# Performance work log

Measured on AMD Instinct MI355X. Metric: run time of the kernel, lower is better.

Reference implementation:

```python
import jax, jax.numpy as jnp
import numpy as np

N = 50000      # nodes
E = 800000     # edges (avg degree 16)
F_IN = 128     # input feature dim
HID = 64       # hidden_channels
HEADS = 2
NEG_SLOPE = 0.2


def setup_inputs() -> dict:
    key = jax.random.key(0)
    ks = jax.random.split(key, 20)
    w = lambda k, shape: jax.random.normal(k, shape, jnp.float32) * 0.1
    inp = {
        "x": jax.random.normal(ks[0], (N, F_IN), jnp.float32),
        "edge_index": jax.random.randint(ks[1], (2, E), 0, N, dtype=jnp.int32),
    }
    # layer specs: (in_dim, heads) ; out per head = HID
    specs = [(F_IN, HEADS), (HID * HEADS, HEADS), (HID * HEADS, HEADS), (HID * HEADS, 1)]
    ki = 2
    for i, (fin, h) in enumerate(specs, 1):
        inp[f"Wl{i}"] = w(ks[ki], (fin, h * HID)); ki += 1
        inp[f"Wr{i}"] = w(ks[ki], (fin, h * HID)); ki += 1
        inp[f"att{i}"] = w(ks[ki], (h, HID)); ki += 1
        inp[f"b{i}"] = jnp.zeros((h * HID,), jnp.float32)
    return inp


def gat_layer(x, src, dst, Wl, Wr, att, b):
    # GATv2Conv: e_ij = att . LeakyReLU(Wl x_j + Wr x_i), softmax over incoming edges of i
    H, C = att.shape
    n = x.shape[0]
    xl = (x @ Wl).reshape(n, H, C)   # source-side transform
    xr = (x @ Wr).reshape(n, H, C)   # target-side transform
    e = jax.nn.leaky_relu(xl[src] + xr[dst], negative_slope=NEG_SLOPE)  # [E,H,C]
    score = jnp.einsum('ehc,hc->eh', e, att)                            # [E,H]
    # segment softmax over destination nodes
    m = jax.ops.segment_max(score, dst, num_segments=n)
    m = jnp.where(jnp.isfinite(m), m, 0.0)  # nodes with no in-edges
    ex = jnp.exp(score - m[dst])
    den = jax.ops.segment_sum(ex, dst, num_segments=n)
    alpha = ex / (den[dst] + 1e-16)                                     # [E,H]
    out = jax.ops.segment_sum(xl[src] * alpha[:, :, None], dst, num_segments=n)  # [N,H,C]
    return out.reshape(n, H * C) + b


def reference(x, edge_index, Wl1, Wr1, att1, b1, Wl2, Wr2, att2, b2,
              Wl3, Wr3, att3, b3, Wl4, Wr4, att4, b4):
    src, dst = edge_index[0], edge_index[1]
    x = jax.nn.relu(gat_layer(x, src, dst, Wl1, Wr1, att1, b1))
    x = jax.nn.relu(gat_layer(x, src, dst, Wl2, Wr2, att2, b2))
    x = jax.nn.relu(gat_layer(x, src, dst, Wl3, Wr3, att3, b3))
    return gat_layer(x, src, dst, Wl4, Wr4, att4, b4)  # [N, HID]
```

## Files before the change

kernel.cpp:

```cpp
#include <hip/hip_runtime.h>
#include <hip/hip_fp16.h>
#include <math.h>
#include <limits.h>

#define FIN 128
#define NEG_SLOPE 0.2f

typedef _Float16 f16x8 __attribute__((ext_vector_type(8)));
typedef float f32x4 __attribute__((ext_vector_type(4)));
typedef float f32x2 __attribute__((ext_vector_type(2)));

static __device__ __forceinline__ f32x2 pk_add(f32x2 a, f32x2 b) {
    f32x2 d; asm("v_pk_add_f32 %0, %1, %2" : "=v"(d) : "v"(a), "v"(b)); return d;
}
static __device__ __forceinline__ f32x2 pk_fma(f32x2 a, f32x2 b, f32x2 c) {
    f32x2 d; asm("v_pk_fma_f32 %0, %1, %2, %3" : "=v"(d) : "v"(a), "v"(b), "v"(c)); return d;
}

static __device__ __forceinline__ f32x2 h2f2x(unsigned int u) {
    __half2 h = *reinterpret_cast<__half2*>(&u);
    float2 f = __half22float2(h);
    return (f32x2){f.x, f.y};
}

template <int CTRL>
static __device__ __forceinline__ float dpp_add(float x) {
    int t = __builtin_amdgcn_update_dpp(0, __builtin_bit_cast(int, x), CTRL, 0xF, 0xF, true);
    return x + __builtin_bit_cast(float, t);
}
static __device__ __forceinline__ float reduce8_dpp(float p) {
    p = dpp_add<0xB1>(p);
    p = dpp_add<0x4E>(p);
    p = dpp_add<0x141>(p);
    return p;
}


__global__ void k_hist(const int* __restrict__ dst, int* __restrict__ counts, int E) {
    int e = blockIdx.x * blockDim.x + threadIdx.x;
    if (e < E) atomicAdd(&counts[dst[e]], 1);
}

__global__ void k_scan1(const int* __restrict__ counts, int* __restrict__ incl,
                        int* __restrict__ partial, int n) {
    __shared__ int tmp[1024];
    int tid = threadIdx.x, base = blockIdx.x * 1024;
    int v = (base + tid < n) ? counts[base + tid] : 0;
    tmp[tid] = v;
    __syncthreads();
    for (int off = 1; off < 1024; off <<= 1) {
        int t = (tid >= off) ? tmp[tid - off] : 0;
        __syncthreads();
        tmp[tid] += t;
        __syncthreads();
    }
    if (base + tid < n) incl[base + tid] = tmp[tid];
    if (tid == 1023) partial[blockIdx.x] = tmp[1023];
}

__global__ void k_scan3(const int* __restrict__ counts, const int* __restrict__ incl,
                        const int* __restrict__ partial, int* __restrict__ rowptr,
                        int* __restrict__ nfill, int n, int nb) {
    __shared__ int sbase;
    if (threadIdx.x == 0) {
        int b = 0;
        for (int p = 0; p < (int)blockIdx.x; ++p) b += partial[p];
        sbase = b;
        if ((int)blockIdx.x == nb - 1) {
            int tot = b;
            for (int p = blockIdx.x; p < nb; ++p) tot += partial[p];
            rowptr[n] = tot;
        }
    }
    __syncthreads();
    int i = blockIdx.x * 1024 + threadIdx.x;
    if (i < n) {
        rowptr[i] = sbase + incl[i] - counts[i];
        nfill[i] = 0;
    }
}

__global__ void k_scatter(const int* __restrict__ dst, const int* __restrict__ rowptr,
                          int* __restrict__ nfill, int* __restrict__ colids, int E) {
    int e = blockIdx.x * blockDim.x + threadIdx.x;
    if (e < E) {
        int d = dst[e];
        int pos = atomicAdd(&nfill[d], 1);
        colids[rowptr[d] + pos] = e;
    }
}

__global__ void k_sort(const int* __restrict__ rowptr, const int* __restrict__ colids,
                       const int* __restrict__ esrc, int* __restrict__ colsrc, int n) {
    int node = blockIdx.x * 4 + (threadIdx.x >> 6);
    int lane = threadIdx.x & 63;
    if (node >= n) return;
    int s = rowptr[node], e = rowptr[node + 1];
    int d = e - s;
    if (d <= 0) return;
    if (d <= 64) {
        int v = (lane < d) ? colids[s + lane] : INT_MAX;
        int rank = 0;
        for (int j = 0; j < d; ++j) {
            int vj = __shfl(v, j, 64);
            rank += (vj < v) ? 1 : 0;
        }
        if (lane < d) colsrc[s + rank] = esrc[v];
    } else {
        if (lane == 0) {
            int last = -1;
            for (int k = 0; k < d; ++k) {
                int best = INT_MAX;
                for (int j = s; j < e; ++j) {
                    int id = colids[j];
                    if (id > last && id < best) best = id;
                }
                colsrc[s + k] = esrc[best];
                last = best;
            }
        }
    }
}


struct WprepArgs {
    const float* Wl[4];
    const float* Wr[4];
    __half* Wz[4];
};

__global__ void k_wprep_all(WprepArgs a) {
    int b = blockIdx.x;
    int layer = (b < 16) ? 0 : (b < 32) ? 1 : (b < 48) ? 2 : 3;
    int base = layer * 16;
    int HC = (layer == 3) ? 64 : 128;
    int NT = 2 * HC / 16;
    int tid = (b - base) * 256 + threadIdx.x;
    int l = tid & 63, c = tid >> 6;
    int ks = c / NT, nt = c % NT;
    int col = nt * 16 + (l & 15);
    int kbase = ks * 32 + ((l >> 4) << 3);
    const float* W = (col < HC) ? (a.Wl[layer] + col) : (a.Wr[layer] + (col - HC));
    __half h[8];
#pragma unroll
    for (int j = 0; j < 8; ++j) h[j] = __float2half(W[(size_t)(kbase + j) * HC]);
    *(uint4*)&a.Wz[layer][(size_t)tid * 8] = *(const uint4*)h;
}


template <int HC, bool CVT>
__global__ void __launch_bounds__(256) k_gemm_mfma(
        const void* __restrict__ Ain, const __half* __restrict__ Wz,
        __half* __restrict__ xl, float* __restrict__ xr, int n) {
    constexpr int NT = 2 * HC / 16;
    const int l = threadIdx.x & 63;
    const int wid = threadIdx.x >> 6;
    const int r0 = (blockIdx.x * 4 + wid) * 16;
    if (r0 >= n) return;
    const int m = l & 15, kb = l >> 4;
    const int ra = min(r0 + m, n - 1);
    const f16x8* Bz = (const f16x8*)Wz;

    f32x4 acc[NT];
#pragma unroll
    for (int nt = 0; nt < NT; ++nt) acc[nt] = (f32x4){0.f, 0.f, 0.f, 0.f};

#pragma unroll
    for (int ks = 0; ks < 4; ++ks) {
        f16x8 a;
        if (CVT) {
            const float* Af = (const float*)Ain + (size_t)ra * FIN + kb * 8 + ks * 32;
            float4 f0 = *(const float4*)Af;
            float4 f1 = *(const float4*)(Af + 4);
            a[0] = (_Float16)f0.x; a[1] = (_Float16)f0.y;
            a[2] = (_Float16)f0.z; a[3] = (_Float16)f0.w;
            a[4] = (_Float16)f1.x; a[5] = (_Float16)f1.y;
            a[6] = (_Float16)f1.z; a[7] = (_Float16)f1.w;
        } else {
            a = *(const f16x8*)((const _Float16*)Ain + (size_t)ra * FIN + kb * 8 + ks * 32);
        }
#pragma unroll
        for (int nt = 0; nt < NT; ++nt) {
            f16x8 b = Bz[(ks * NT + nt) * 64 + l];
            acc[nt] = __builtin_amdgcn_mfma_f32_16x16x32_f16(a, b, acc[nt], 0, 0, 0);
        }
    }

    const int rb = r0 + kb * 4;
#pragma unroll
    for (int nt = 0; nt < NT; ++nt) {
        int c = nt * 16 + m;
        if (nt < NT / 2) {
#pragma unroll
            for (int r = 0; r < 4; ++r) {
                int row = rb + r;
                if (row < n) xl[(size_t)row * HC + c] = __float2half(acc[nt][r]);
            }
        } else {
            int cd = c - HC;
#pragma unroll
            for (int r = 0; r < 4; ++r) {
                int row = rb + r;
                if (row < n) xr[(size_t)row * HC + cd] = acc[nt][r];
            }
        }
    }
}


template <bool RELU>
__global__ void __launch_bounds__(256) k_fused2(
        const __half* __restrict__ xlh, const float* __restrict__ xr,
        const int* __restrict__ rowptr, const int* __restrict__ colsrc,
        const float* __restrict__ attc, const float* __restrict__ bias,
        __half* __restrict__ out, int N) {
    const int lane = threadIdx.x & 63;
    const int g = lane >> 4;
    const int s = lane & 15;
    const int c0 = s * 8;
    int i = blockIdx.x * 4 + (threadIdx.x >> 6);
    const int stride = gridDim.x * 4;
    const float L2E = 1.4426950408889634f;

    f32x2 a6[4], a4[4];
    {
        float4 a0 = *(const float4*)&attc[c0];
        float4 a1 = *(const float4*)&attc[c0 + 4];
        float t[8] = {a0.x, a0.y, a0.z, a0.w, a1.x, a1.y, a1.z, a1.w};
#pragma unroll
        for (int k = 0; k < 4; ++k) {
            a6[k] = (f32x2){0.6f * L2E * t[2 * k], 0.6f * L2E * t[2 * k + 1]};
            a4[k] = (f32x2){0.4f * L2E * t[2 * k], 0.4f * L2E * t[2 * k + 1]};
        }
    }

    for (; i < N; i += stride) {
        f32x2 xrv[4];
        {
            float4 r0 = *(const float4*)&xr[(size_t)i * 128 + c0];
            float4 r1 = *(const float4*)&xr[(size_t)i * 128 + c0 + 4];
            xrv[0] = (f32x2){r0.x, r0.y}; xrv[1] = (f32x2){r0.z, r0.w};
            xrv[2] = (f32x2){r1.x, r1.y}; xrv[3] = (f32x2){r1.z, r1.w};
        }
        const int st = rowptr[i], en = rowptr[i + 1];
        float den = 0.f;
        f32x2 acc[4];
#pragma unroll
        for (int k = 0; k < 4; ++k) acc[k] = (f32x2){0.f, 0.f};

        if (st < en) {
            const int em1 = en - 1;
            int i0 = colsrc[min(st + g, em1)];
            int i1 = colsrc[min(st + 4 + g, em1)];
            uint4 w0 = *(const uint4*)(xlh + ((size_t)i0 << 7) + c0);
            uint4 w1 = *(const uint4*)(xlh + ((size_t)i1 << 7) + c0);
            i0 = colsrc[min(st + 8 + g, em1)];
            i1 = colsrc[min(st + 12 + g, em1)];
            for (int j = st; j < en; j += 8) {
                uint4 n0 = *(const uint4*)(xlh + ((size_t)i0 << 7) + c0);
                uint4 n1 = *(const uint4*)(xlh + ((size_t)i1 << 7) + c0);
                i0 = colsrc[min(j + 16 + g, em1)];
                i1 = colsrc[min(j + 20 + g, em1)];

#pragma unroll
                for (int q = 0; q < 2; ++q) {
                    const uint4 w = q ? w1 : w0;
                    f32x2 xv[4];
                    xv[0] = h2f2x(w.x); xv[1] = h2f2x(w.y);
                    xv[2] = h2f2x(w.z); xv[3] = h2f2x(w.w);
                    f32x2 sc = (f32x2){0.f, 0.f};
#pragma unroll
                    for (int k = 0; k < 4; ++k) {
                        f32x2 u = pk_add(xv[k], xrv[k]);
                        sc = pk_fma(u, a6[k], sc);
                        f32x2 ua = {__builtin_fabsf(u.x), __builtin_fabsf(u.y)};
                        sc = pk_fma(ua, a4[k], sc);
                    }
                    float p = reduce8_dpp(sc.x + sc.y);
                    p = (j + q * 4 + g < en) ? p : -INFINITY;
                    float pe = exp2f(p);
                    den += pe;
                    f32x2 pe2 = (f32x2){pe, pe};
#pragma unroll
                    for (int k = 0; k < 4; ++k) acc[k] = pk_fma(pe2, xv[k], acc[k]);
                }
                w0 = n0; w1 = n1;
            }
        }

#pragma unroll
        for (int off = 16; off <= 32; off <<= 1) {
            den += __shfl_xor(den, off, 64);
#pragma unroll
            for (int k = 0; k < 4; ++k) {
                acc[k].x += __shfl_xor(acc[k].x, off, 64);
                acc[k].y += __shfl_xor(acc[k].y, off, 64);
            }
        }

        if (g == 0) {
            float4 b0 = *(const float4*)&bias[c0];
            float4 b1 = *(const float4*)&bias[c0 + 4];
            float bv[8] = {b0.x, b0.y, b0.z, b0.w, b1.x, b1.y, b1.z, b1.w};
            float inv = 1.f / (den + 1e-16f);
            __half hb[8];
#pragma unroll
            for (int k = 0; k < 8; ++k) {
                float av = (k & 1) ? acc[k >> 1].y : acc[k >> 1].x;
                float o = fmaf(av, inv, bv[k]);
                if (RELU) o = fmaxf(o, 0.f);
                hb[k] = __float2half(o);
            }
            *(uint4*)&out[(size_t)i * 128 + c0] = *(const uint4*)hb;
        }
    }
}


__global__ void __launch_bounds__(256) k_fused1(
        const __half* __restrict__ xlh, const float* __restrict__ xr,
        const int* __restrict__ rowptr, const int* __restrict__ colsrc,
        const float* __restrict__ attc, const float* __restrict__ bias,
        float* __restrict__ out, int N) {
    const int lane = threadIdx.x & 63;
    const int g = lane >> 3;
    const int s = lane & 7;
    const int c0 = s * 8;
    int i = blockIdx.x * 4 + (threadIdx.x >> 6);
    const int stride = gridDim.x * 4;
    const float L2E = 1.4426950408889634f;

    f32x2 a6[4], a4[4];
    {
        float4 a0 = *(const float4*)&attc[c0];
        float4 a1 = *(const float4*)&attc[c0 + 4];
        float t[8] = {a0.x, a0.y, a0.z, a0.w, a1.x, a1.y, a1.z, a1.w};
#pragma unroll
        for (int k = 0; k < 4; ++k) {
            a6[k] = (f32x2){0.6f * L2E * t[2 * k], 0.6f * L2E * t[2 * k + 1]};
            a4[k] = (f32x2){0.4f * L2E * t[2 * k], 0.4f * L2E * t[2 * k + 1]};
        }
    }

    for (; i < N; i += stride) {
        f32x2 xrv[4];
        {
            float4 r0 = *(const float4*)&xr[(size_t)i * 64 + c0];
            float4 r1 = *(const float4*)&xr[(size_t)i * 64 + c0 + 4];
            xrv[0] = (f32x2){r0.x, r0.y}; xrv[1] = (f32x2){r0.z, r0.w};
            xrv[2] = (f32x2){r1.x, r1.y}; xrv[3] = (f32x2){r1.z, r1.w};
        }
        const int st = rowptr[i], en = rowptr[i + 1];
        float den = 0.f;
        f32x2 acc[4];
#pragma unroll
        for (int k = 0; k < 4; ++k) acc[k] = (f32x2){0.f, 0.f};

        if (st < en) {
            const int em1 = en - 1;
            int i0 = colsrc[min(st + g, em1)];
            int i1 = colsrc[min(st + 8 + g, em1)];
            uint4 w0 = *(const uint4*)(xlh + ((size_t)i0 << 6) + c0);
            uint4 w1 = *(const uint4*)(xlh + ((size_t)i1 << 6) + c0);
            i0 = colsrc[min(st + 16 + g, em1)];
            i1 = colsrc[min(st + 24 + g, em1)];
            for (int j = st; j < en; j += 16) {
                uint4 n0 = *(const uint4*)(xlh + ((size_t)i0 << 6) + c0);
                uint4 n1 = *(const uint4*)(xlh + ((size_t)i1 << 6) + c0);
                i0 = colsrc[min(j + 32 + g, em1)];
                i1 = colsrc[min(j + 40 + g, em1)];

#pragma unroll
                for (int q = 0; q < 2; ++q) {
                    const uint4 w = q ? w1 : w0;
                    f32x2 xv[4];
                    xv[0] = h2f2x(w.x); xv[1] = h2f2x(w.y);
                    xv[2] = h2f2x(w.z); xv[3] = h2f2x(w.w);
                    f32x2 sc = (f32x2){0.f, 0.f};
#pragma unroll
                    for (int k = 0; k < 4; ++k) {
                        f32x2 u = pk_add(xv[k], xrv[k]);
                        sc = pk_fma(u, a6[k], sc);
                        f32x2 ua = {__builtin_fabsf(u.x), __builtin_fabsf(u.y)};
                        sc = pk_fma(ua, a4[k], sc);
                    }
                    float p = reduce8_dpp(sc.x + sc.y);
                    p = (j + q * 8 + g < en) ? p : -INFINITY;
                    float pe = exp2f(p);
                    den += pe;
                    f32x2 pe2 = (f32x2){pe, pe};
#pragma unroll
                    for (int k = 0; k < 4; ++k) acc[k] = pk_fma(pe2, xv[k], acc[k]);
                }
                w0 = n0; w1 = n1;
            }
        }

#pragma unroll
        for (int off = 8; off <= 32; off <<= 1) {
            den += __shfl_xor(den, off, 64);
#pragma unroll
            for (int k = 0; k < 4; ++k) {
                acc[k].x += __shfl_xor(acc[k].x, off, 64);
                acc[k].y += __shfl_xor(acc[k].y, off, 64);
            }
        }

        if (g == 0) {
            float4 b0 = *(const float4*)&bias[c0];
            float4 b1 = *(const float4*)&bias[c0 + 4];
            float bv[8] = {b0.x, b0.y, b0.z, b0.w, b1.x, b1.y, b1.z, b1.w};
            float inv = 1.f / (den + 1e-16f);
            float o[8];
#pragma unroll
            for (int k = 0; k < 8; ++k) {
                float av = (k & 1) ? acc[k >> 1].y : acc[k >> 1].x;
                o[k] = fmaf(av, inv, bv[k]);
            }
            *(float4*)&out[(size_t)i * 64 + c0] = make_float4(o[0], o[1], o[2], o[3]);
            *(float4*)&out[(size_t)i * 64 + c0 + 4] = make_float4(o[4], o[5], o[6], o[7]);
        }
    }
}


static inline size_t align_up(size_t v, size_t a) { return (v + a - 1) & ~(a - 1); }

extern "C" void kernel_launch(void* const* d_in, const int* in_sizes, int n_in,
                              void* d_out, int out_size, void* d_ws, size_t ws_size,
                              hipStream_t stream) {
    const float* x = (const float*)d_in[0];
    const int* ei = (const int*)d_in[1];
    const int N = in_sizes[0] / FIN;
    const int E = in_sizes[1] / 2;
    const int* esrc = ei;
    const int* edst = ei + E;

    const float* Wl1 = (const float*)d_in[2];
    const float* Wr1 = (const float*)d_in[3];
    const float* att1 = (const float*)d_in[4];
    const float* b1 = (const float*)d_in[5];
    const float* Wl2 = (const float*)d_in[6];
    const float* Wr2 = (const float*)d_in[7];
    const float* att2 = (const float*)d_in[8];
    const float* b2 = (const float*)d_in[9];
    const float* Wl3 = (const float*)d_in[10];
    const float* Wr3 = (const float*)d_in[11];
    const float* att3 = (const float*)d_in[12];
    const float* b3 = (const float*)d_in[13];
    const float* Wl4 = (const float*)d_in[14];
    const float* Wr4 = (const float*)d_in[15];
    const float* att4 = (const float*)d_in[16];
    const float* b4 = (const float*)d_in[17];

    const int nb = (N + 1023) / 1024;

    size_t off = 0;
    char* w = (char*)d_ws;
    auto alloc = [&](size_t bytes) {
        char* p = w + off;
        off = align_up(off + bytes, 256);
        return p;
    };
    int* rowptr = (int*)alloc((size_t)(N + 1) * 4);
    int* nfill = (int*)alloc((size_t)N * 4);
    int* incl = (int*)alloc((size_t)N * 4);
    int* partial = (int*)alloc(1024 * 4);
    int* colids = (int*)alloc((size_t)E * 4);
    int* colsrc = (int*)alloc((size_t)E * 4);
    __half* xb16 = (__half*)alloc((size_t)N * FIN * 2);
    __half* xlh = (__half*)alloc((size_t)N * FIN * 2);
    float* xr = (float*)alloc((size_t)N * FIN * 4);
    __half* Wz1 = (__half*)alloc(65536);
    __half* Wz2 = (__half*)alloc(65536);
    __half* Wz3 = (__half*)alloc(65536);
    __half* Wz4 = (__half*)alloc(32768);
    if (off > ws_size) return;

    hipMemsetAsync(nfill, 0, (size_t)N * 4, stream);
    k_hist<<<(E + 255) / 256, 256, 0, stream>>>(edst, nfill, E);
    k_scan1<<<nb, 1024, 0, stream>>>(nfill, incl, partial, N);
    k_scan3<<<nb, 1024, 0, stream>>>(nfill, incl, partial, rowptr, nfill, N, nb);
    k_scatter<<<(E + 255) / 256, 256, 0, stream>>>(edst, rowptr, nfill, colids, E);
    k_sort<<<(N + 3) / 4, 256, 0, stream>>>(rowptr, colids, esrc, colsrc, N);

    WprepArgs wa;
    wa.Wl[0] = Wl1; wa.Wl[1] = Wl2; wa.Wl[2] = Wl3; wa.Wl[3] = Wl4;
    wa.Wr[0] = Wr1; wa.Wr[1] = Wr2; wa.Wr[2] = Wr3; wa.Wr[3] = Wr4;
    wa.Wz[0] = Wz1; wa.Wz[1] = Wz2; wa.Wz[2] = Wz3; wa.Wz[3] = Wz4;
    k_wprep_all<<<56, 256, 0, stream>>>(wa);

    const int gg = (N + 63) / 64;
    const int gf = min(2048, (N + 3) / 4);

    k_gemm_mfma<128, true><<<gg, 256, 0, stream>>>(x, Wz1, xlh, xr, N);
    k_fused2<true><<<gf, 256, 0, stream>>>(xlh, xr, rowptr, colsrc, att1, b1, xb16, N);
    k_gemm_mfma<128, false><<<gg, 256, 0, stream>>>(xb16, Wz2, xlh, xr, N);
    k_fused2<true><<<gf, 256, 0, stream>>>(xlh, xr, rowptr, colsrc, att2, b2, xb16, N);
    k_gemm_mfma<128, false><<<gg, 256, 0, stream>>>(xb16, Wz3, xlh, xr, N);
    k_fused2<true><<<gf, 256, 0, stream>>>(xlh, xr, rowptr, colsrc, att3, b3, xb16, N);
    k_gemm_mfma<64, false><<<gg, 256, 0, stream>>>(xb16, Wz4, xlh, xr, N);
    k_fused1<<<gf, 256, 0, stream>>>(xlh, xr, rowptr, colsrc, att4, b4, (float*)d_out, N);
}
```

Measured before the change: 394.6 us.

## Deepen gather prefetch, drop edge clamping via padded colsrc, launch one block per node group

In the two-head aggregation kernel, the gather pipeline is extended from one to two stages of xlh row loads in flight. In both kernels the min(...,en-1) clamps on colsrc indices are removed. To keep the look-ahead reads in bounds, colsrc is padded with 64 zeroed entries at the end, so out-of-segment indices read real neighbor rows (or row 0) and rely on the -INFINITY mask. The fused kernels' grid is no longer capped at 2048 blocks and now launches one block per four nodes. The aim is more memory-level parallelism and less index arithmetic, at the cost of extra registers and wasted gathers for low-degree nodes.

```diff
diff --git a/kernel.cpp b/kernel.cpp
--- a/kernel.cpp
+++ b/kernel.cpp
@@ -249,18 +249,17 @@
         for (int k = 0; k < 4; ++k) acc[k] = (f32x2){0.f, 0.f};
 
         if (st < en) {
-            const int em1 = en - 1;
-            int i0 = colsrc[min(st + g, em1)];
-            int i1 = colsrc[min(st + 4 + g, em1)];
-            uint4 w0 = *(const uint4*)(xlh + ((size_t)i0 << 7) + c0);
-            uint4 w1 = *(const uint4*)(xlh + ((size_t)i1 << 7) + c0);
-            i0 = colsrc[min(st + 8 + g, em1)];
-            i1 = colsrc[min(st + 12 + g, em1)];
+            uint4 w0 = *(const uint4*)(xlh + ((size_t)colsrc[st + g] << 7) + c0);
+            uint4 w1 = *(const uint4*)(xlh + ((size_t)colsrc[st + 4 + g] << 7) + c0);
+            uint4 w2 = *(const uint4*)(xlh + ((size_t)colsrc[st + 8 + g] << 7) + c0);
+            uint4 w3 = *(const uint4*)(xlh + ((size_t)colsrc[st + 12 + g] << 7) + c0);
+            int i0 = colsrc[st + 16 + g];
+            int i1 = colsrc[st + 20 + g];
             for (int j = st; j < en; j += 8) {
                 uint4 n0 = *(const uint4*)(xlh + ((size_t)i0 << 7) + c0);
                 uint4 n1 = *(const uint4*)(xlh + ((size_t)i1 << 7) + c0);
-                i0 = colsrc[min(j + 16 + g, em1)];
-                i1 = colsrc[min(j + 20 + g, em1)];
+                i0 = colsrc[j + 24 + g];
+                i1 = colsrc[j + 28 + g];
 
 #pragma unroll
                 for (int q = 0; q < 2; ++q) {
@@ -284,7 +283,7 @@
 #pragma unroll
                     for (int k = 0; k < 4; ++k) acc[k] = pk_fma(pe2, xv[k], acc[k]);
                 }
-                w0 = n0; w1 = n1;
+                w0 = w2; w1 = w3; w2 = n0; w3 = n1;
             }
         }
 
@@ -357,18 +356,15 @@
         for (int k = 0; k < 4; ++k) acc[k] = (f32x2){0.f, 0.f};
 
         if (st < en) {
-            const int em1 = en - 1;
-            int i0 = colsrc[min(st + g, em1)];
-            int i1 = colsrc[min(st + 8 + g, em1)];
-            uint4 w0 = *(const uint4*)(xlh + ((size_t)i0 << 6) + c0);
-            uint4 w1 = *(const uint4*)(xlh + ((size_t)i1 << 6) + c0);
-            i0 = colsrc[min(st + 16 + g, em1)];
-            i1 = colsrc[min(st + 24 + g, em1)];
+            uint4 w0 = *(const uint4*)(xlh + ((size_t)colsrc[st + g] << 6) + c0);
+            uint4 w1 = *(const uint4*)(xlh + ((size_t)colsrc[st + 8 + g] << 6) + c0);
+            int i0 = colsrc[st + 16 + g];
+            int i1 = colsrc[st + 24 + g];
             for (int j = st; j < en; j += 16) {
                 uint4 n0 = *(const uint4*)(xlh + ((size_t)i0 << 6) + c0);
                 uint4 n1 = *(const uint4*)(xlh + ((size_t)i1 << 6) + c0);
-                i0 = colsrc[min(j + 32 + g, em1)];
-                i1 = colsrc[min(j + 40 + g, em1)];
+                i0 = colsrc[j + 32 + g];
+                i1 = colsrc[j + 40 + g];
 
 #pragma unroll
                 for (int q = 0; q < 2; ++q) {
@@ -467,7 +463,7 @@
     int* incl = (int*)alloc((size_t)N * 4);
     int* partial = (int*)alloc(1024 * 4);
     int* colids = (int*)alloc((size_t)E * 4);
-    int* colsrc = (int*)alloc((size_t)E * 4);
+    int* colsrc = (int*)alloc((size_t)(E + 64) * 4);
     __half* xb16 = (__half*)alloc((size_t)N * FIN * 2);
     __half* xlh = (__half*)alloc((size_t)N * FIN * 2);
     float* xr = (float*)alloc((size_t)N * FIN * 4);
@@ -478,6 +474,7 @@
     if (off > ws_size) return;
 
     hipMemsetAsync(nfill, 0, (size_t)N * 4, stream);
+    hipMemsetAsync(colsrc + E, 0, 64 * 4, stream);
     k_hist<<<(E + 255) / 256, 256, 0, stream>>>(edst, nfill, E);
     k_scan1<<<nb, 1024, 0, stream>>>(nfill, incl, partial, N);
     k_scan3<<<nb, 1024, 0, stream>>>(nfill, incl, partial, rowptr, nfill, N, nb);
@@ -491,7 +488,7 @@
     k_wprep_all<<<56, 256, 0, stream>>>(wa);
 
     const int gg = (N + 63) / 64;
-    const int gf = min(2048, (N + 3) / 4);
+    const int gf = (N + 3) / 4;
 
     k_gemm_mfma<128, true><<<gg, 256, 0, stream>>>(x, Wz1, xlh, xr, N);
     k_fused2<true><<<gf, 256, 0, stream>>>(xlh, xr, rowptr, colsrc, att1, b1, xb16, N);
```

Result: no change. 388.0 us (-1.7%).
